# Kernel optimization log

Measured on AMD Instinct MI355X. Metric: run time of the kernel, lower is better.

Reference implementation:

```python
import jax, jax.numpy as jnp
import numpy as np

B, C, H, W = 16, 256, 64, 64
K = 3
K2 = K * K
EPS = 1e-5


def setup_inputs() -> dict:
    key = jax.random.key(0)
    ks = jax.random.split(key, 5)
    scale_r = 1.0 / np.sqrt(C)
    return {
        "X": jax.random.normal(ks[0], (B, C, H, W), dtype=jnp.float32),
        "w_reduce": jax.random.normal(ks[1], (C, C), dtype=jnp.float32) * scale_r,
        "b_reduce": jax.random.normal(ks[2], (C,), dtype=jnp.float32) * 0.01,
        "gamma": jnp.ones((C,), dtype=jnp.float32),
        "beta": jnp.zeros((C,), dtype=jnp.float32),
        "w_span": jax.random.normal(ks[3], (C * K2, C), dtype=jnp.float32) * scale_r,
        "b_span": jax.random.normal(ks[4], (C * K2,), dtype=jnp.float32) * 0.01,
    }


def _unfold3x3(X):
    # torch nn.Unfold(3, padding=1, stride=1): patches (B, C, 9, H, W),
    # kernel positions row-major, channel slowest -- matches torch ordering.
    b, c, h, w = X.shape
    Xp = jnp.pad(X, ((0, 0), (0, 0), (1, 1), (1, 1)))
    return jnp.stack(
        [Xp[:, :, i:i + h, j:j + w] for i in range(K) for j in range(K)], axis=2
    )  # (B, C, 9, H, W)


def reference(X, w_reduce, b_reduce, gamma, beta, w_span, b_span):
    # stride=1 -> AvgPool is Identity. reduce: 1x1 conv C -> C (reduction=1)
    Wr = jnp.einsum('bchw,oc->bohw', X, w_reduce) + b_reduce[None, :, None, None]
    # BatchNorm2d (training mode: biased batch stats over B,H,W) + ReLU
    mean = Wr.mean(axis=(0, 2, 3))
    var = Wr.var(axis=(0, 2, 3))
    Wn = (Wr - mean[None, :, None, None]) * jax.lax.rsqrt(var[None, :, None, None] + EPS)
    Wn = jax.nn.relu(Wn * gamma[None, :, None, None] + beta[None, :, None, None])
    # span: 1x1 conv C -> g*k^2 (g = C since group_ch = 1)
    Ker = jnp.einsum('bchw,oc->bohw', Wn, w_span) + b_span[None, :, None, None]
    Ker = Ker.reshape(B, C, K2, H * W)  # (b, g, k^2, h*w); group_ch broadcast dim implied
    patches = _unfold3x3(X).reshape(B, C, K2, H * W)
    out = (patches * Ker).sum(axis=2)  # fused multiply-reduce over k^2
    return out.reshape(B, C, H, W)
```

## Files before the change

### kernel.cpp

```cpp
#include <hip/hip_runtime.h>
#include <stdint.h>


typedef __attribute__((ext_vector_type(4))) float f32x4;
typedef __attribute__((ext_vector_type(8))) short s16x8;
typedef __attribute__((ext_vector_type(8))) __bf16 bf16x8;

#define WAITV(N) asm volatile("s_waitcnt vmcnt(" #N ")" ::: "memory")
#define WAITL0   asm volatile("s_waitcnt lgkmcnt(0)" ::: "memory")
#define PIN()    asm volatile("" ::: "memory")
#define BAR()    do { PIN(); __builtin_amdgcn_s_barrier(); PIN(); } while (0)

__device__ __forceinline__ float bf2f(uint16_t u){
  union { uint32_t i; float f; } v; v.i = ((uint32_t)u) << 16; return v.f;
}
__device__ __forceinline__ uint16_t f2bf(float f){
  union { float f; uint32_t i; } v; v.f = f;
  return (uint16_t)((v.i + 0x7fffu + ((v.i >> 16) & 1u)) >> 16);
}

template <typename V>
__device__ __forceinline__ auto mfma16x16x32(V a, V b, f32x4 c, int)
    -> decltype(__builtin_amdgcn_mfma_f32_16x16x32_bf16(a, b, c, 0, 0, 0)) {
  return __builtin_amdgcn_mfma_f32_16x16x32_bf16(a, b, c, 0, 0, 0);
}
template <typename V>
__device__ __forceinline__ f32x4 mfma16x16x32(V a, V b, f32x4 c, long) {
  bf16x8 aa = __builtin_bit_cast(bf16x8, a);
  bf16x8 bb = __builtin_bit_cast(bf16x8, b);
  return __builtin_amdgcn_mfma_f32_16x16x32_bf16(aa, bb, c, 0, 0, 0);
}

typedef uint32_t u32_g __attribute__((address_space(1)));
typedef uint32_t u32_l __attribute__((address_space(3)));
__device__ __forceinline__ void glds16(const void* g, void* l){
  __builtin_amdgcn_global_load_lds((const u32_g*)g, (u32_l*)l, 16, 0, 0);
}

__global__ __launch_bounds__(256) void prep_weights(
    const float* __restrict__ wred, const float* __restrict__ wsp,
    uint16_t* __restrict__ wrt, uint16_t* __restrict__ wspt){
  int id = blockIdx.x * 256 + threadIdx.x;
  union { uint4 v; uint16_t h[8]; } u;
  if (id < 8192){
    int ks = id >> 10;
    int o  = (id >> 2) & 255;
    int j0 = (id & 3) * 8;
    const float* s = wred + o * 256 + ks * 32 + j0;
    #pragma unroll
    for (int i = 0; i < 8; i++) u.h[i] = f2bf(s[i]);
    *(uint4*)(wrt + ((size_t)(ks * 256 + o) * 32 + j0)) = u.v;
  } else {
    int c16 = id - 8192;
    int j0  = (c16 & 3) * 8;
    int row = c16 >> 2;
    int phys = row % 144;
    int mtks = row / 144;
    int mt = mtks & 15, ks = mtks >> 4;
    int g = phys & 15, k2 = phys >> 4;
    int sg = mt * 144 + g * 9 + k2;
    const float* s = wsp + (size_t)sg * 256 + ks * 32 + j0;
    #pragma unroll
    for (int i = 0; i < 8; i++) u.h[i] = f2bf(s[i]);
    *(uint4*)(wspt + ((size_t)row * 32 + j0)) = u.v;
  }
}

__global__ __launch_bounds__(256) void k1_reduce_gemm(
    const float* __restrict__ X, const uint16_t* __restrict__ wrt,
    const float* __restrict__ bred, uint16_t* __restrict__ Wr,
    float* __restrict__ part){
  const int pt = blockIdx.x, mt = blockIdx.y, b = blockIdx.z;
  const int p0 = pt * 128, o0 = mt * 128;
  __shared__ __align__(16) uint16_t Al[2][128*32];
  __shared__ __align__(16) uint16_t Bl[2][128*32];
  __shared__ float redS[256], redQ[256];
  const int t = threadIdx.x;
  const int wv = t >> 6, lane = t & 63, q = lane >> 4, l = lane & 15;
  const int wm = wv >> 1, wn = wv & 1;
  const int c2 = (t & 15) * 2, seg = t >> 4;
  f32x4 acc[4][4] = {};
  union { float f[8]; float4 v[2]; } v0, v1;

  auto stageA = [&](int ks, int buf){
    const char* src = (const char*)(wrt + ((size_t)ks * 256 + o0) * 32);
    char* dst = (char*)(&Al[buf][0]);
    for (int cc = wv; cc < 8; cc += 4)
      glds16(src + cc*1024 + lane*16, dst + cc*1024);
  };
  auto loadB = [&](int ks){
    const float* s0 = X + ((size_t)(b * 256 + ks * 32 + c2)) * 4096 + p0 + seg * 8;
    const float* s1 = s0 + 4096;
    v0.v[0] = *(const float4*)(s0 + 0);
    v0.v[1] = *(const float4*)(s0 + 4);
    v1.v[0] = *(const float4*)(s1 + 0);
    v1.v[1] = *(const float4*)(s1 + 4);
  };
  auto writeB = [&](int buf){
    uint16_t* dst = &Bl[buf][(seg * 8) * 32 + c2];
    #pragma unroll
    for (int i = 0; i < 8; i++){
      uint32_t pk = (uint32_t)f2bf(v0.f[i]) | ((uint32_t)f2bf(v1.f[i]) << 16);
      *(uint32_t*)(dst + (size_t)i * 32) = pk;
    }
  };

  stageA(0, 0); loadB(0); writeB(0);
  __syncthreads();
  int cur = 0;
  for (int ks = 0; ks < 8; ks++){
    if (ks < 7){ stageA(ks + 1, cur ^ 1); loadB(ks + 1); }
    s16x8 af[4], bfv[4];
    #pragma unroll
    for (int mi = 0; mi < 4; mi++)
      af[mi] = *(const s16x8*)(&Al[cur][(wm*64 + mi*16 + l)*32 + q*8]);
    #pragma unroll
    for (int ni = 0; ni < 4; ni++)
      bfv[ni] = *(const s16x8*)(&Bl[cur][(wn*64 + ni*16 + l)*32 + q*8]);
    #pragma unroll
    for (int mi = 0; mi < 4; mi++)
      #pragma unroll
      for (int ni = 0; ni < 4; ni++)
        acc[mi][ni] = mfma16x16x32(af[mi], bfv[ni], acc[mi][ni], 0);
    if (ks < 7) writeB(cur ^ 1);
    __syncthreads();
    cur ^= 1;
  }
  float ssum[4][4] = {}, ssq[4][4] = {};
  #pragma unroll
  for (int mi = 0; mi < 4; mi++){
    int o = o0 + wm*64 + mi*16 + q*4;
    float4 br = *(const float4*)(bred + o);
    int slab = o >> 5, orem = o & 31;
    #pragma unroll
    for (int ni = 0; ni < 4; ni++){
      int p = p0 + wn*64 + ni*16 + l;
      f32x4 v = acc[mi][ni];
      float e0 = v[0] + br.x, e1 = v[1] + br.y, e2 = v[2] + br.z, e3 = v[3] + br.w;
      ssum[mi][0] += e0; ssq[mi][0] += e0*e0;
      ssum[mi][1] += e1; ssq[mi][1] += e1*e1;
      ssum[mi][2] += e2; ssq[mi][2] += e2*e2;
      ssum[mi][3] += e3; ssq[mi][3] += e3*e3;
      uint32_t lo = (uint32_t)f2bf(e0) | ((uint32_t)f2bf(e1) << 16);
      uint32_t hi = (uint32_t)f2bf(e2) | ((uint32_t)f2bf(e3) << 16);
      uint2 pk; pk.x = lo; pk.y = hi;
      *(uint2*)(Wr + ((size_t)((b*8 + slab)*4096 + p)) * 32 + orem) = pk;
    }
  }
  #pragma unroll
  for (int mi = 0; mi < 4; mi++)
    #pragma unroll
    for (int j = 0; j < 4; j++){
      #pragma unroll
      for (int off = 1; off < 16; off <<= 1){
        ssum[mi][j] += __shfl_xor(ssum[mi][j], off);
        ssq[mi][j]  += __shfl_xor(ssq[mi][j],  off);
      }
    }
  if (l == 0){
    #pragma unroll
    for (int mi = 0; mi < 4; mi++)
      #pragma unroll
      for (int j = 0; j < 4; j++){
        int ch_local = wm*64 + mi*16 + q*4 + j;
        redS[ch_local*2 + wn] = ssum[mi][j];
        redQ[ch_local*2 + wn] = ssq[mi][j];
      }
  }
  __syncthreads();
  {
    int ch_local = t >> 1, m = t & 1;
    float val = m ? (redQ[ch_local*2] + redQ[ch_local*2+1])
                  : (redS[ch_local*2] + redS[ch_local*2+1]);
    int ch = o0 + ch_local;
    int idx = pt*16 + b;
    part[((size_t)ch*512 + idx)*2 + m] = val;
  }
}

__global__ __launch_bounds__(64) void bn_final(
    const float* __restrict__ part, const float* __restrict__ gamma,
    const float* __restrict__ beta, float* __restrict__ coeffs){
  int c = blockIdx.x, t = threadIdx.x;
  float s = 0.f, sq = 0.f;
  const float* p = part + (size_t)c * 1024;
  #pragma unroll
  for (int i = 0; i < 8; i++){
    float2 v = *(const float2*)(p + (t*8 + i)*2);
    s += v.x; sq += v.y;
  }
  #pragma unroll
  for (int off = 1; off < 64; off <<= 1){
    s  += __shfl_xor(s,  off);
    sq += __shfl_xor(sq, off);
  }
  if (t == 0){
    const float inv = 1.0f / 65536.0f;
    float mean = s * inv;
    float var  = sq * inv - mean * mean;
    float rstd = rsqrtf(var + 1e-5f);
    float A = gamma[c] * rstd;
    float Bc = beta[c] - mean * A;
    coeffs[2*c] = A; coeffs[2*c+1] = Bc;
  }
}

__global__ __launch_bounds__(256) void bn_apply(uint16_t* __restrict__ Wr,
                                                const float* __restrict__ coeffs){
  __shared__ float cf[512];
  cf[threadIdx.x]       = coeffs[threadIdx.x];
  cf[threadIdx.x + 256] = coeffs[threadIdx.x + 256];
  __syncthreads();
  #pragma unroll
  for (int it = 0; it < 4; it++){
    size_t c16 = (size_t)blockIdx.x * 256 + threadIdx.x + (size_t)it * (2048u*256u);
    uint16_t* pch = Wr + c16 * 8;
    int sj = (int)((c16 >> 14) & 7);
    int j0 = (int)(c16 & 3) * 8;
    union { uint4 v; uint16_t h[8]; } u;
    u.v = *(const uint4*)pch;
    #pragma unroll
    for (int i = 0; i < 8; i++){
      int cch = sj * 32 + j0 + i;
      float v = bf2f(u.h[i]);
      v = fmaf(v, cf[2*cch], cf[2*cch+1]);
      v = fmaxf(v, 0.f);
      u.h[i] = f2bf(v);
    }
    *(uint4*)pch = u.v;
  }
}

__global__ __launch_bounds__(256, 2) void k3_span_inv(
    const uint16_t* __restrict__ Wn, const uint16_t* __restrict__ wspt,
    const float* __restrict__ bspan, const float* __restrict__ X,
    float* __restrict__ out){
  const int orig = blockIdx.x;
  const int wgid = (orig & 7) * 512 + (orig >> 3);
  const int mt = wgid & 15, pt = (wgid >> 4) & 15, b = wgid >> 8;
  const int p0 = pt * 256;
  __shared__ __align__(16) uint16_t Al[2][144*32];
  __shared__ float Xl[16*6*66];
  __shared__ float bsp[144];
  const int t = threadIdx.x;
  const int wv = t >> 6, lane = t & 63, q = lane >> 4, l = lane & 15;
  const int qs = q ^ ((l >> 1) & 3);
  if (t < 144){
    int g = t & 15, k2 = t >> 4;
    bsp[t] = bspan[mt*144 + g*9 + k2];
  }
  f32x4 acc[9][4] = {};

  const int lsw = ((lane >> 2) << 6) + ((((lane & 3) ^ ((lane >> 3) & 3))) << 4);
  const char* Abase = (const char*)(wspt + (size_t)mt * (144*32));
  const size_t AslabB = (size_t)16 * 144 * 64;
  const uint16_t* Bb = Wn + (((size_t)(b*8))*4096 + p0 + wv*64 + l)*32 + q*8;
  const size_t BslabE = (size_t)4096 * 32;

  auto stageA = [&](int ks, int buf){
    const char* asrc = Abase + (size_t)ks * AslabB + lsw;
    char* adst = (char*)(&Al[buf][0]);
    glds16(asrc + (size_t)wv*1024,     adst + wv*1024);
    glds16(asrc + (size_t)(wv+4)*1024, adst + (wv+4)*1024);
    if (wv == 0) glds16(asrc + 8*1024, adst + 8*1024);
  };

  s16x8 bb[2][4];
  stageA(0, 0);
  PIN();
  #pragma unroll
  for (int ni = 0; ni < 4; ni++) bb[0][ni] = *(const s16x8*)(Bb + 0*BslabE + (size_t)ni*512);
  #pragma unroll
  for (int ni = 0; ni < 4; ni++) bb[1][ni] = *(const s16x8*)(Bb + 1*BslabE + (size_t)ni*512);
  PIN();
  WAITV(8);
  BAR();

  #pragma unroll
  for (int ks = 0; ks < 8; ks++){
    if (ks < 7) stageA(ks + 1, (ks + 1) & 1);
    PIN();
    __builtin_amdgcn_s_setprio(1);
    #pragma unroll
    for (int mi = 0; mi < 9; mi++){
      s16x8 af = *(const s16x8*)(&Al[ks & 1][(mi*16 + l)*32 + qs*8]);
      acc[mi][0] = mfma16x16x32(af, bb[ks & 1][0], acc[mi][0], 0);
      acc[mi][1] = mfma16x16x32(af, bb[ks & 1][1], acc[mi][1], 0);
      acc[mi][2] = mfma16x16x32(af, bb[ks & 1][2], acc[mi][2], 0);
      acc[mi][3] = mfma16x16x32(af, bb[ks & 1][3], acc[mi][3], 0);
    }
    __builtin_amdgcn_s_setprio(0);
    if (ks < 6){
      #pragma unroll
      for (int ni = 0; ni < 4; ni++)
        bb[ks & 1][ni] = *(const s16x8*)(Bb + (size_t)(ks+2)*BslabE + (size_t)ni*512);
    }
    if (ks < 7){
      if (ks < 6) { WAITV(4); } else { WAITV(0); }
      WAITL0;
      BAR();
    }
  }

  if (t < 192){
    int ch = t / 12, rr = t % 12, r = rr >> 1;
    Xl[(ch*6 + r)*66 + (rr & 1)*65] = 0.f;
  }
  #pragma unroll
  for (int i = 0; i < 6; i++){
    int v = t + i*256;
    int ch = v / 96, rem = v % 96;
    int r = rem >> 4, c4 = (rem & 15) * 4;
    int hr = pt*4 - 1 + r;
    float4 val = make_float4(0.f, 0.f, 0.f, 0.f);
    if (hr >= 0 && hr < 64)
      val = *(const float4*)(X + ((size_t)(b*256 + mt*16 + ch))*4096 + hr*64 + c4);
    float* dst = &Xl[(ch*6 + r)*66 + 1 + c4];
    dst[0] = val.x; dst[1] = val.y; dst[2] = val.z; dst[3] = val.w;
  }
  WAITL0;
  BAR();

  const int h = pt*4 + wv;
  #pragma unroll
  for (int reg = 0; reg < 4; reg++){
    const int g  = q*4 + reg;
    const int gg = mt*16 + g;
    float* Oc = out + ((size_t)(b*256 + gg) * 64 + h) * 64;
    float bs[9];
    #pragma unroll
    for (int k2 = 0; k2 < 9; k2++) bs[k2] = bsp[k2*16 + g];
    const float* Xr0 = &Xl[(g*6 + wv)*66 + l];
    float rr4[4] = {0.f, 0.f, 0.f, 0.f};
    #pragma unroll
    for (int dh = 0; dh < 3; dh++){
      const float* Xr = Xr0 + dh*66;
      #pragma unroll
      for (int ni = 0; ni < 4; ni++){
        #pragma unroll
        for (int dw = 0; dw < 3; dw++){
          const int k2 = dh*3 + dw;
          rr4[ni] = fmaf(acc[k2][ni][reg] + bs[k2], Xr[ni*16 + dw], rr4[ni]);
        }
      }
    }
    #pragma unroll
    for (int ni = 0; ni < 4; ni++) Oc[ni*16 + l] = rr4[ni];
  }
}

extern "C" void kernel_launch(void* const* d_in, const int* in_sizes, int n_in,
                              void* d_out, int out_size, void* d_ws, size_t ws_size,
                              hipStream_t stream) {
  const float* X     = (const float*)d_in[0];
  const float* wred  = (const float*)d_in[1];
  const float* bred  = (const float*)d_in[2];
  const float* gamma = (const float*)d_in[3];
  const float* beta  = (const float*)d_in[4];
  const float* wsp   = (const float*)d_in[5];
  const float* bsp   = (const float*)d_in[6];
  float* out = (float*)d_out;

  char* ws = (char*)d_ws;
  uint16_t* Wr   = (uint16_t*)(ws);
  uint16_t* wrt  = (uint16_t*)(ws + 33554432);
  uint16_t* wspt = (uint16_t*)(ws + 33554432 + 131072);
  float* part    = (float*)(ws + 33554432 + 131072 + 1179648);
  float* coeffs  = (float*)(ws + 33554432 + 131072 + 1179648 + 1048576);
  if (ws_size < (size_t)(33554432 + 131072 + 1179648 + 1048576 + 2048)) return;

  prep_weights<<<320, 256, 0, stream>>>(wred, wsp, wrt, wspt);
  k1_reduce_gemm<<<dim3(32, 2, 16), 256, 0, stream>>>(X, wrt, bred, Wr, part);
  bn_final<<<256, 64, 0, stream>>>(part, gamma, beta, coeffs);
  bn_apply<<<2048, 256, 0, stream>>>(Wr, coeffs);
  k3_span_inv<<<4096, 256, 0, stream>>>(Wr, wspt, bsp, X, out);
}
```

Baseline: 152.6 us.

## Prefetch X halo during span GEMM and transpose MFMA output for vector stores

```diff
diff --git a/kernel.cpp b/kernel.cpp
--- a/kernel.cpp
+++ b/kernel.cpp
@@ -15,8 +15,8 @@
   union { uint32_t i; float f; } v; v.i = ((uint32_t)u) << 16; return v.f;
 }
 __device__ __forceinline__ uint16_t f2bf(float f){
-  union { float f; uint32_t i; } v; v.f = f;
-  return (uint16_t)((v.i + 0x7fffu + ((v.i >> 16) & 1u)) >> 16);
+  __bf16 h = (__bf16)f;
+  return __builtin_bit_cast(uint16_t, h);
 }
 
 template <typename V>
@@ -240,7 +240,7 @@
   const int mt = wgid & 15, pt = (wgid >> 4) & 15, b = wgid >> 8;
   const int p0 = pt * 256;
   __shared__ __align__(16) uint16_t Al[2][144*32];
-  __shared__ float Xl[16*6*66];
+  __shared__ __align__(16) float Xl[16*6*68];
   __shared__ float bsp[144];
   const int t = threadIdx.x;
   const int wv = t >> 6, lane = t & 63, q = lane >> 4, l = lane & 15;
@@ -249,6 +249,10 @@
     int g = t & 15, k2 = t >> 4;
     bsp[t] = bspan[mt*144 + g*9 + k2];
   }
+  if (t < 192){
+    int ch = t / 12, rr = t % 12, r = rr >> 1;
+    Xl[(ch*6 + r)*68 + (rr & 1)*65] = 0.f;
+  }
   f32x4 acc[9][4] = {};
 
   const int lsw = ((lane >> 2) << 6) + ((((lane & 3) ^ ((lane >> 3) & 3))) << 4);
@@ -266,6 +270,7 @@
   };
 
   s16x8 bb[2][4];
+  float4 xv[6];
   stageA(0, 0);
   PIN();
   #pragma unroll
@@ -280,14 +285,43 @@
   for (int ks = 0; ks < 8; ks++){
     if (ks < 7) stageA(ks + 1, (ks + 1) & 1);
     PIN();
+    if (ks == 0){
+      #pragma unroll
+      for (int i = 0; i < 6; i++){
+        int v = t + i*256;
+        int ch = v / 96, rem = v - ch*96;
+        int r = rem >> 4, c4 = (rem & 15) * 4;
+        int hr = pt*4 - 1 + r;
+        int hrc = min(max(hr, 0), 63);
+        xv[i] = *(const float4*)(X + ((size_t)(b*256 + mt*16 + ch))*4096 + hrc*64 + c4);
+      }
+      PIN();
+    }
+    if (ks == 1){
+      #pragma unroll
+      for (int i = 0; i < 6; i++){
+        int v = t + i*256;
+        int ch = v / 96, rem = v - ch*96;
+        int r = rem >> 4, c4 = (rem & 15) * 4;
+        int hr = pt*4 - 1 + r;
+        bool ok = (hr >= 0) && (hr < 64);
+        float4 val = xv[i];
+        int d = (ch*6 + r)*68 + 1 + c4;
+        Xl[d]   = ok ? val.x : 0.f;
+        Xl[d+1] = ok ? val.y : 0.f;
+        Xl[d+2] = ok ? val.z : 0.f;
+        Xl[d+3] = ok ? val.w : 0.f;
+      }
+      PIN();
+    }
     __builtin_amdgcn_s_setprio(1);
     #pragma unroll
     for (int mi = 0; mi < 9; mi++){
       s16x8 af = *(const s16x8*)(&Al[ks & 1][(mi*16 + l)*32 + qs*8]);
-      acc[mi][0] = mfma16x16x32(af, bb[ks & 1][0], acc[mi][0], 0);
-      acc[mi][1] = mfma16x16x32(af, bb[ks & 1][1], acc[mi][1], 0);
-      acc[mi][2] = mfma16x16x32(af, bb[ks & 1][2], acc[mi][2], 0);
-      acc[mi][3] = mfma16x16x32(af, bb[ks & 1][3], acc[mi][3], 0);
+      acc[mi][0] = mfma16x16x32(bb[ks & 1][0], af, acc[mi][0], 0);
+      acc[mi][1] = mfma16x16x32(bb[ks & 1][1], af, acc[mi][1], 0);
+      acc[mi][2] = mfma16x16x32(bb[ks & 1][2], af, acc[mi][2], 0);
+      acc[mi][3] = mfma16x16x32(bb[ks & 1][3], af, acc[mi][3], 0);
     }
     __builtin_amdgcn_s_setprio(0);
     if (ks < 6){
@@ -302,50 +336,38 @@
     }
   }
 
-  if (t < 192){
-    int ch = t / 12, rr = t % 12, r = rr >> 1;
-    Xl[(ch*6 + r)*66 + (rr & 1)*65] = 0.f;
-  }
-  #pragma unroll
-  for (int i = 0; i < 6; i++){
-    int v = t + i*256;
-    int ch = v / 96, rem = v % 96;
-    int r = rem >> 4, c4 = (rem & 15) * 4;
-    int hr = pt*4 - 1 + r;
-    float4 val = make_float4(0.f, 0.f, 0.f, 0.f);
-    if (hr >= 0 && hr < 64)
-      val = *(const float4*)(X + ((size_t)(b*256 + mt*16 + ch))*4096 + hr*64 + c4);
-    float* dst = &Xl[(ch*6 + r)*66 + 1 + c4];
-    dst[0] = val.x; dst[1] = val.y; dst[2] = val.z; dst[3] = val.w;
-  }
-  WAITL0;
-  BAR();
-
+  float bs[9];
+  #pragma unroll
+  for (int k2 = 0; k2 < 9; k2++) bs[k2] = bsp[k2*16 + l];
+  #pragma unroll
+  for (int k2 = 0; k2 < 9; k2++)
+    #pragma unroll
+    for (int ni = 0; ni < 4; ni++){
+      acc[k2][ni][0] += bs[k2]; acc[k2][ni][1] += bs[k2];
+      acc[k2][ni][2] += bs[k2]; acc[k2][ni][3] += bs[k2];
+    }
   const int h = pt*4 + wv;
-  #pragma unroll
-  for (int reg = 0; reg < 4; reg++){
-    const int g  = q*4 + reg;
-    const int gg = mt*16 + g;
-    float* Oc = out + ((size_t)(b*256 + gg) * 64 + h) * 64;
-    float bs[9];
-    #pragma unroll
-    for (int k2 = 0; k2 < 9; k2++) bs[k2] = bsp[k2*16 + g];
-    const float* Xr0 = &Xl[(g*6 + wv)*66 + l];
-    float rr4[4] = {0.f, 0.f, 0.f, 0.f};
+  const int gg = mt*16 + l;
+  float* Oc = out + ((size_t)(b*256 + gg) * 64 + h) * 64;
+  const float* Xrow = &Xl[(l*6 + wv) * 68];
+  #pragma unroll
+  for (int ni = 0; ni < 4; ni++){
+    f32x4 res = {0.f, 0.f, 0.f, 0.f};
     #pragma unroll
     for (int dh = 0; dh < 3; dh++){
-      const float* Xr = Xr0 + dh*66;
-      #pragma unroll
-      for (int ni = 0; ni < 4; ni++){
+      const float* xp = Xrow + dh*68 + ni*16 + q*4;
+      f32x4 xa = *(const f32x4*)xp;
+      float2 xb = *(const float2*)(xp + 4);
+      float x[6] = {xa[0], xa[1], xa[2], xa[3], xb.x, xb.y};
+      #pragma unroll
+      for (int dw = 0; dw < 3; dw++){
+        const int k2 = dh*3 + dw;
         #pragma unroll
-        for (int dw = 0; dw < 3; dw++){
-          const int k2 = dh*3 + dw;
-          rr4[ni] = fmaf(acc[k2][ni][reg] + bs[k2], Xr[ni*16 + dw], rr4[ni]);
-        }
-      }
-    }
-    #pragma unroll
-    for (int ni = 0; ni < 4; ni++) Oc[ni*16 + l] = rr4[ni];
+        for (int reg = 0; reg < 4; reg++)
+          res[reg] = fmaf(acc[k2][ni][reg], x[reg + dw], res[reg]);
+      }
+    }
+    *(f32x4*)(Oc + ni*16 + q*4) = res;
   }
 }
 
```

Measured after the change: 134.6 us. -11.8%, faster.
